# Kernel tuning notes

Measured on AMD Instinct MI355X. Metric: run time of the kernel, lower is better.

The kernel has to match this reference:

```python
import jax, jax.numpy as jnp
import numpy as np

B, T, C, H = 16, 2048, 192, 64

def setup_inputs() -> dict:
    key = jax.random.key(0)
    k1, k2, k3, k4 = jax.random.split(key, 4)
    x = jax.random.normal(k1, (B, T, C), dtype=jnp.float32)
    Wq = jax.random.normal(k2, (C, H), dtype=jnp.float32) * (C ** -0.5)
    Wk = jax.random.normal(k3, (C, H), dtype=jnp.float32) * (C ** -0.5)
    Wv = jax.random.normal(k4, (C, H), dtype=jnp.float32) * (C ** -0.5)
    return {"x": x, "Wq": Wq, "Wk": Wk, "Wv": Wv}

def reference(x, Wq, Wk, Wv):
    # One head of causal self-attention (dropout in eval mode / identity).
    q = x @ Wq                       # [B, T, H]
    k = x @ Wk                       # [B, T, H]
    v = x @ Wv                       # [B, T, H]
    scale = q.shape[-1] ** -0.5
    wei = jnp.einsum('bth,bsh->bts', q, k) * scale   # [B, T, T]
    t = wei.shape[-1]
    causal = jnp.tril(jnp.ones((t, t), dtype=bool))  # tril mask
    wei = jnp.where(causal, wei, -jnp.inf)
    wei = jax.nn.softmax(wei, axis=-1)
    out = jnp.einsum('bts,bsh->bth', wei, v)         # [B, T, H]
    return out
```

## Files before the change

kernel.cpp:

```cpp
#include <hip/hip_runtime.h>

#define B 16
#define T 2048
#define C 192
#define H 64

typedef __bf16 bf16x8 __attribute__((ext_vector_type(8)));
typedef __bf16 bf16x4 __attribute__((ext_vector_type(4)));
typedef float  f32x4  __attribute__((ext_vector_type(4)));

#define MFMA(a, b, c) __builtin_amdgcn_mfma_f32_16x16x32_bf16(a, b, c, 0, 0, 0)

#define SM_BIAS 24.0f

__global__ __launch_bounds__(256) void wtrans_kernel(
    const float* __restrict__ Wq, const float* __restrict__ Wk,
    const float* __restrict__ Wv, __bf16* __restrict__ wt)
{
    const int idx = blockIdx.x * 256 + threadIdx.x;
    const int n = idx / C;
    const int k = idx - n * C;
    const float* W = (n < 64) ? Wq : (n < 128) ? Wk : Wv;
    const int nc = n & 63;
    wt[n * C + k] = (__bf16)W[k * H + nc];
}

__global__ __launch_bounds__(256) void qkv_mfma_kernel(
    const float* __restrict__ x, const __bf16* __restrict__ wt,
    __bf16* __restrict__ qb, __bf16* __restrict__ kb, __bf16* __restrict__ vt)
{
    __shared__ __bf16 Ws[2][192][40];
    __shared__ __bf16 tile[64][72];

    const int tid  = threadIdx.x;
    const int w    = tid >> 6;
    const int lid  = tid & 15;
    const int quad = (tid & 63) >> 4;
    const int m0   = blockIdx.x * 64 + w * 16;

    const float* xrow = x + (size_t)(m0 + lid) * C + quad * 8;
    float4 a0[6], a1[6];
    #pragma unroll
    for (int kc = 0; kc < 6; kc++) {
        a0[kc] = *(const float4*)(xrow + kc * 32);
        a1[kc] = *(const float4*)(xrow + kc * 32 + 4);
    }
    bf16x8 af[6];
    #pragma unroll
    for (int kc = 0; kc < 6; kc++) {
        af[kc][0] = (__bf16)a0[kc].x; af[kc][1] = (__bf16)a0[kc].y;
        af[kc][2] = (__bf16)a0[kc].z; af[kc][3] = (__bf16)a0[kc].w;
        af[kc][4] = (__bf16)a1[kc].x; af[kc][5] = (__bf16)a1[kc].y;
        af[kc][6] = (__bf16)a1[kc].z; af[kc][7] = (__bf16)a1[kc].w;
    }

    bf16x8 wpf[3];
    auto prefW = [&](int kc) {
        #pragma unroll
        for (int i = 0; i < 3; i++) {
            const int p = i * 256 + tid;
            wpf[i] = *(const bf16x8*)(wt + (p >> 2) * C + kc * 32 + (p & 3) * 8);
        }
    };

    f32x4 acc[12] = {};
    prefW(0);
    int cur = 0;
    for (int kc = 0; kc < 6; kc++) {
        #pragma unroll
        for (int i = 0; i < 3; i++) {
            const int p = i * 256 + tid;
            *(bf16x8*)&Ws[cur][p >> 2][(p & 3) * 8] = wpf[i];
        }
        __syncthreads();
        if (kc < 5) prefW(kc + 1);
        #pragma unroll
        for (int nt = 0; nt < 12; nt++) {
            const bf16x8 bfr = *(const bf16x8*)&Ws[cur][nt * 16 + lid][quad * 8];
            acc[nt] = MFMA(af[kc], bfr, acc[nt]);
        }
        cur ^= 1;
    }

    #pragma unroll
    for (int nt = 0; nt < 8; nt++) {
        const int n = nt * 16 + lid;
        __bf16* dst = (n < 64) ? qb : kb;
        const int col = n & 63;
        const float scale = (n < 64) ? 0.1803368801111204f : 1.0f;
        #pragma unroll
        for (int r = 0; r < 4; r++) {
            const int row = m0 + quad * 4 + r;
            dst[(size_t)row * H + col] = (__bf16)(acc[nt][r] * scale);
        }
    }

    #pragma unroll
    for (int nt = 8; nt < 12; nt++) {
        const int col = (nt - 8) * 16 + lid;
        #pragma unroll
        for (int r = 0; r < 4; r++)
            tile[w * 16 + quad * 4 + r][col] = (__bf16)(acc[nt][r]);
    }
    __syncthreads();

    const int bb = blockIdx.x >> 5;
    const int t0 = (blockIdx.x & 31) << 6;
    #pragma unroll
    for (int it = 0; it < 2; ++it) {
        const int h   = it * 32 + (tid >> 3);
        const int tl0 = (tid & 7) * 8;
        bf16x8 d;
        #pragma unroll
        for (int j = 0; j < 8; j++) d[j] = tile[tl0 + j][h];
        *(bf16x8*)(vt + ((size_t)(bb * H + h)) * T + t0 + tl0) = d;
    }
}

__global__ __launch_bounds__(512, 2) void attn_kernel(
    const __bf16* __restrict__ qb,
    const __bf16* __restrict__ kb,
    const __bf16* __restrict__ vt,
    float* __restrict__ out)
{
    __shared__ __bf16 Kb[2][2][64][72];
    __shared__ __bf16 Vb[2][2][64][68];

    const int tid  = threadIdx.x;
    const int wv   = tid >> 6;
    const int grp  = wv >> 2;
    const int w    = wv & 3;
    const int lid  = tid & 15;
    const int quad = (tid & 63) >> 4;

    const int b   = blockIdx.x & 15;
    const int pr  = blockIdx.x >> 4;
    const int qtH = 31 - pr, qtL = pr;
    const int nchH = qtH + 1;
    const int ntot = 33;
    const size_t bbase = (size_t)b * T;

    const int qH = (qtH << 6) + w * 16;
    const int qL = (qtL << 6) + w * 16;

    const __bf16* qrH = qb + (bbase + qH + lid) * H + quad * 8;
    const bf16x8 qfH0 = *(const bf16x8*)(qrH);
    const bf16x8 qfH1 = *(const bf16x8*)(qrH + 32);
    const __bf16* qrL = qb + (bbase + qL + lid) * H + quad * 8;
    const bf16x8 qfL0 = *(const bf16x8*)(qrL);
    const bf16x8 qfL1 = *(const bf16x8*)(qrL + 32);

    const __bf16* kgb = kb + bbase * H;
    const __bf16* vgb = vt + (size_t)b * H * T;

    const int ra = tid >> 3, ca = (tid & 7) * 8;

    auto keyof = [&](int i) {
        if (i > ntot - 1) i = ntot - 1;
        return (i < nchH ? i : i - nchH) << 6;
    };

    bf16x8 kr[2], vr2[2];
    auto prefetch = [&](int s) {
        #pragma unroll
        for (int g = 0; g < 2; g++) {
            const int key0 = keyof(2 * s + g);
            kr[g]  = *(const bf16x8*)(kgb + (size_t)(key0 + ra) * H + ca);
            vr2[g] = *(const bf16x8*)(vgb + (size_t)ra * T + key0 + ca);
        }
    };

    f32x4 OH[4] = {}, OL[4] = {};
    float lsH = 0.f, lsL = 0.f;

    auto doChunk = [&](f32x4 (&O)[4], float& ls, bf16x8 cq0, bf16x8 cq1,
                       int cqw, int key0, int cur) {
        const __bf16 (*Kc)[72] = Kb[cur][grp];
        const __bf16 (*Vc)[68] = Vb[cur][grp];
        bf16x8 kf[8];
        #pragma unroll
        for (int j = 0; j < 4; j++) {
            kf[2*j]   = *(const bf16x8*)&Kc[j * 16 + lid][quad * 8];
            kf[2*j+1] = *(const bf16x8*)&Kc[j * 16 + lid][32 + quad * 8];
        }
        bf16x8 bv0[4], bv1[4];
        #pragma unroll
        for (int ht = 0; ht < 4; ht++) {
            const __bf16* vr_ = &Vc[ht * 16 + lid][quad * 4];
            ((bf16x4*)&bv0[ht])[0] = *(const bf16x4*)(vr_);
            ((bf16x4*)&bv0[ht])[1] = *(const bf16x4*)(vr_ + 16);
            ((bf16x4*)&bv1[ht])[0] = *(const bf16x4*)(vr_ + 32);
            ((bf16x4*)&bv1[ht])[1] = *(const bf16x4*)(vr_ + 48);
        }
        bf16x8 af0, af1;
        const bool boundary = (key0 + 63 > cqw);
        #pragma unroll
        for (int j = 0; j < 4; j++) {
            f32x4 sS = {-SM_BIAS, -SM_BIAS, -SM_BIAS, -SM_BIAS};
            sS = MFMA(kf[2*j], cq0, sS);
            sS = MFMA(kf[2*j+1], cq1, sS);
            if (boundary) {
                #pragma unroll
                for (int r = 0; r < 4; r++)
                    if (key0 + j * 16 + quad * 4 + r > cqw + lid) sS[r] = -1e30f;
            }
            #pragma unroll
            for (int r = 0; r < 4; r++) {
                const float p = __builtin_amdgcn_exp2f(sS[r]);
                ls += p;
                if      (j == 0) af0[r]     = (__bf16)p;
                else if (j == 1) af0[4 + r] = (__bf16)p;
                else if (j == 2) af1[r]     = (__bf16)p;
                else             af1[4 + r] = (__bf16)p;
            }
        }
        #pragma unroll
        for (int ht = 0; ht < 4; ht++) {
            O[ht] = MFMA(af0, bv0[ht], O[ht]);
            O[ht] = MFMA(af1, bv1[ht], O[ht]);
        }
    };

    prefetch(0);
    int cur = 0;
    for (int s = 0; s < 17; s++) {
        *(bf16x8*)&Kb[cur][0][ra][ca] = kr[0];
        *(bf16x8*)&Kb[cur][1][ra][ca] = kr[1];
        *(bf16x8*)&Vb[cur][0][ra][ca] = vr2[0];
        *(bf16x8*)&Vb[cur][1][ra][ca] = vr2[1];
        __syncthreads();
        if (s + 1 < 17) prefetch(s + 1);

        const int i = 2 * s + grp;
        if (i < ntot) {
            const bool heavy = (i < nchH);
            const int key0 = (heavy ? i : i - nchH) << 6;
            if (heavy) doChunk(OH, lsH, qfH0, qfH1, qH, key0, cur);
            else       doChunk(OL, lsL, qfL0, qfL1, qL, key0, cur);
        }
        cur ^= 1;
    }

    __syncthreads();
    float* sO = (float*)&Kb[0][0][0][0];
    float* sL = (float*)&Vb[0][0][0][0];

    float lh = lsH; lh += __shfl_xor(lh, 16, 64); lh += __shfl_xor(lh, 32, 64);
    float ll = lsL; ll += __shfl_xor(ll, 16, 64); ll += __shfl_xor(ll, 32, 64);

    if (grp == 1) {
        #pragma unroll
        for (int ht = 0; ht < 4; ht++)
            #pragma unroll
            for (int r = 0; r < 4; r++) {
                sO[((0 * 4 + w) * 16 + quad * 4 + r) * 64 + ht * 16 + lid] = OH[ht][r];
                sO[((1 * 4 + w) * 16 + quad * 4 + r) * 64 + ht * 16 + lid] = OL[ht][r];
            }
        if ((tid & 63) < 16) {
            sL[(0 * 4 + w) * 16 + lid] = lh;
            sL[(1 * 4 + w) * 16 + lid] = ll;
        }
    }
    __syncthreads();
    if (grp == 0) {
        lh += sL[(0 * 4 + w) * 16 + lid];
        ll += sL[(1 * 4 + w) * 16 + lid];
        #pragma unroll
        for (int ht = 0; ht < 4; ht++)
            #pragma unroll
            for (int r = 0; r < 4; r++) {
                const float LrH = __shfl(lh, quad * 4 + r, 16);
                const float vH = OH[ht][r]
                    + sO[((0 * 4 + w) * 16 + quad * 4 + r) * 64 + ht * 16 + lid];
                out[(bbase + qH + quad * 4 + r) * H + ht * 16 + lid] = vH / LrH;

                const float LrL = __shfl(ll, quad * 4 + r, 16);
                const float vL = OL[ht][r]
                    + sO[((1 * 4 + w) * 16 + quad * 4 + r) * 64 + ht * 16 + lid];
                out[(bbase + qL + quad * 4 + r) * H + ht * 16 + lid] = vL / LrL;
            }
    }
}

extern "C" void kernel_launch(void* const* d_in, const int* in_sizes, int n_in,
                              void* d_out, int out_size, void* d_ws, size_t ws_size,
                              hipStream_t stream)
{
    const float* x  = (const float*)d_in[0];
    const float* Wq = (const float*)d_in[1];
    const float* Wk = (const float*)d_in[2];
    const float* Wv = (const float*)d_in[3];

    const size_t BTH = (size_t)B * T * H;
    __bf16* qbuf = (__bf16*)d_ws;
    __bf16* kbuf = qbuf + BTH;
    __bf16* vtb  = kbuf + BTH;
    __bf16* wt   = vtb + BTH;
    float* outp = (float*)d_out;

    wtrans_kernel<<<(C * 3 * H) / 256, 256, 0, stream>>>(Wq, Wk, Wv, wt);
    qkv_mfma_kernel<<<B * T / 64, 256, 0, stream>>>(x, wt, qbuf, kbuf, vtb);
    attn_kernel<<<B * T / 128, 512, 0, stream>>>(qbuf, kbuf, vtb, outp);
}
```

Baseline: 105.7 us.

## Split QKV projection into 32-row blocks with 2x2 wave layout

The QKV projection kernel now handles 32 rows per block instead of 64. Its four waves form a 2x2 grid over rows and output columns, so each wave holds 6 accumulators instead of 12. This doubles the grid size and cuts register and LDS use, which should raise occupancy and spread the projection across more CUs. The cost is single-buffered weight tiles with an extra barrier per k-step, and every x row block now reloads the full weight matrix.

```diff
diff --git a/kernel.cpp b/kernel.cpp
--- a/kernel.cpp
+++ b/kernel.cpp
@@ -25,33 +25,31 @@
     wt[n * C + k] = (__bf16)W[k * H + nc];
 }
 
-__global__ __launch_bounds__(256) void qkv_mfma_kernel(
+__global__ __launch_bounds__(256, 4) void qkv_mfma_kernel(
     const float* __restrict__ x, const __bf16* __restrict__ wt,
     __bf16* __restrict__ qb, __bf16* __restrict__ kb, __bf16* __restrict__ vt)
 {
-    __shared__ __bf16 Ws[2][192][40];
-    __shared__ __bf16 tile[64][72];
+    __shared__ __bf16 Ws[192][40];
+    __shared__ __bf16 tile[32][72];
 
     const int tid  = threadIdx.x;
     const int w    = tid >> 6;
+    const int rw   = w & 1;
+    const int cw   = w >> 1;
     const int lid  = tid & 15;
     const int quad = (tid & 63) >> 4;
-    const int m0   = blockIdx.x * 64 + w * 16;
+    const int m0   = blockIdx.x * 32 + rw * 16;
 
     const float* xrow = x + (size_t)(m0 + lid) * C + quad * 8;
-    float4 a0[6], a1[6];
-    #pragma unroll
-    for (int kc = 0; kc < 6; kc++) {
-        a0[kc] = *(const float4*)(xrow + kc * 32);
-        a1[kc] = *(const float4*)(xrow + kc * 32 + 4);
-    }
     bf16x8 af[6];
     #pragma unroll
     for (int kc = 0; kc < 6; kc++) {
-        af[kc][0] = (__bf16)a0[kc].x; af[kc][1] = (__bf16)a0[kc].y;
-        af[kc][2] = (__bf16)a0[kc].z; af[kc][3] = (__bf16)a0[kc].w;
-        af[kc][4] = (__bf16)a1[kc].x; af[kc][5] = (__bf16)a1[kc].y;
-        af[kc][6] = (__bf16)a1[kc].z; af[kc][7] = (__bf16)a1[kc].w;
+        const float4 a0 = *(const float4*)(xrow + kc * 32);
+        const float4 a1 = *(const float4*)(xrow + kc * 32 + 4);
+        af[kc][0] = (__bf16)a0.x; af[kc][1] = (__bf16)a0.y;
+        af[kc][2] = (__bf16)a0.z; af[kc][3] = (__bf16)a0.w;
+        af[kc][4] = (__bf16)a1.x; af[kc][5] = (__bf16)a1.y;
+        af[kc][6] = (__bf16)a1.z; af[kc][7] = (__bf16)a1.w;
     }
 
     bf16x8 wpf[3];
@@ -63,58 +61,54 @@
         }
     };
 
-    f32x4 acc[12] = {};
+    f32x4 acc[6] = {};
     prefW(0);
-    int cur = 0;
     for (int kc = 0; kc < 6; kc++) {
         #pragma unroll
         for (int i = 0; i < 3; i++) {
             const int p = i * 256 + tid;
-            *(bf16x8*)&Ws[cur][p >> 2][(p & 3) * 8] = wpf[i];
+            *(bf16x8*)&Ws[p >> 2][(p & 3) * 8] = wpf[i];
         }
         __syncthreads();
         if (kc < 5) prefW(kc + 1);
         #pragma unroll
-        for (int nt = 0; nt < 12; nt++) {
-            const bf16x8 bfr = *(const bf16x8*)&Ws[cur][nt * 16 + lid][quad * 8];
-            acc[nt] = MFMA(af[kc], bfr, acc[nt]);
-        }
-        cur ^= 1;
+        for (int j = 0; j < 6; j++) {
+            const int nt = cw * 6 + j;
+            const bf16x8 bfr = *(const bf16x8*)&Ws[nt * 16 + lid][quad * 8];
+            acc[j] = MFMA(af[kc], bfr, acc[j]);
+        }
+        __syncthreads();
     }
 
     #pragma unroll
-    for (int nt = 0; nt < 8; nt++) {
-        const int n = nt * 16 + lid;
-        __bf16* dst = (n < 64) ? qb : kb;
-        const int col = n & 63;
-        const float scale = (n < 64) ? 0.1803368801111204f : 1.0f;
-        #pragma unroll
-        for (int r = 0; r < 4; r++) {
-            const int row = m0 + quad * 4 + r;
-            dst[(size_t)row * H + col] = (__bf16)(acc[nt][r] * scale);
-        }
-    }
-
+    for (int j = 0; j < 6; j++) {
+        const int nt = cw * 6 + j;
+        const int n  = nt * 16 + lid;
+        if (n < 128) {
+            __bf16* dst = (n < 64) ? qb : kb;
+            const int col = n & 63;
+            const float scale = (n < 64) ? 0.1803368801111204f : 1.0f;
+            #pragma unroll
+            for (int r = 0; r < 4; r++)
+                dst[(size_t)(m0 + quad * 4 + r) * H + col] =
+                    (__bf16)(acc[j][r] * scale);
+        } else {
+            const int col = n - 128;
+            #pragma unroll
+            for (int r = 0; r < 4; r++)
+                tile[rw * 16 + quad * 4 + r][col] = (__bf16)acc[j][r];
+        }
+    }
+    __syncthreads();
+
+    const int bb  = blockIdx.x >> 6;
+    const int t0  = (blockIdx.x & 63) << 5;
+    const int h   = tid >> 2;
+    const int tl0 = (tid & 3) * 8;
+    bf16x8 d;
     #pragma unroll
-    for (int nt = 8; nt < 12; nt++) {
-        const int col = (nt - 8) * 16 + lid;
-        #pragma unroll
-        for (int r = 0; r < 4; r++)
-            tile[w * 16 + quad * 4 + r][col] = (__bf16)(acc[nt][r]);
-    }
-    __syncthreads();
-
-    const int bb = blockIdx.x >> 5;
-    const int t0 = (blockIdx.x & 31) << 6;
-    #pragma unroll
-    for (int it = 0; it < 2; ++it) {
-        const int h   = it * 32 + (tid >> 3);
-        const int tl0 = (tid & 7) * 8;
-        bf16x8 d;
-        #pragma unroll
-        for (int j = 0; j < 8; j++) d[j] = tile[tl0 + j][h];
-        *(bf16x8*)(vt + ((size_t)(bb * H + h)) * T + t0 + tl0) = d;
-    }
+    for (int j = 0; j < 8; j++) d[j] = tile[tl0 + j][h];
+    *(bf16x8*)(vt + ((size_t)(bb * H + h)) * T + t0 + tl0) = d;
 }
 
 __global__ __launch_bounds__(512, 2) void attn_kernel(
@@ -299,6 +293,6 @@
     float* outp = (float*)d_out;
 
     wtrans_kernel<<<(C * 3 * H) / 256, 256, 0, stream>>>(Wq, Wk, Wv, wt);
-    qkv_mfma_kernel<<<B * T / 64, 256, 0, stream>>>(x, wt, qbuf, kbuf, vtb);
+    qkv_mfma_kernel<<<B * T / 32, 256, 0, stream>>>(x, wt, qbuf, kbuf, vtb);
     attn_kernel<<<B * T / 128, 512, 0, stream>>>(qbuf, kbuf, vtb, outp);
 }
```

New measurement: 109.5 us. 1.04x slower.

## Split attention key chunks across four wave groups in 1024-thread blocks

Applied to the files above, without the earlier changes.

Raises the attention block from 512 to 1024 threads, so four wave groups each take one 64-key chunk per step instead of two groups. This cuts the loop from 17 steps to 9 and widens the cross-group reduction of partial outputs and row sums to three extra groups through shared memory. K and V fragments are now loaded from LDS inside the MFMA loops instead of all up front, which lowers register pressure. In exchange the kernel uses more LDS per block, adds a bigger reduction at the end, and still pays a block-wide barrier each step.

```diff
diff --git a/kernel.cpp b/kernel.cpp
--- a/kernel.cpp
+++ b/kernel.cpp
@@ -117,14 +117,16 @@
     }
 }
 
-__global__ __launch_bounds__(512, 2) void attn_kernel(
+#define KB_ELEMS (64 * 72)
+#define VB_ELEMS (64 * 68)
+
+__global__ __launch_bounds__(1024) void attn_kernel(
     const __bf16* __restrict__ qb,
     const __bf16* __restrict__ kb,
     const __bf16* __restrict__ vt,
     float* __restrict__ out)
 {
-    __shared__ __bf16 Kb[2][2][64][72];
-    __shared__ __bf16 Vb[2][2][64][68];
+    __shared__ __align__(16) __bf16 smem[8 * KB_ELEMS + 8 * VB_ELEMS];
 
     const int tid  = threadIdx.x;
     const int wv   = tid >> 6;
@@ -138,7 +140,15 @@
     const int qtH = 31 - pr, qtL = pr;
     const int nchH = qtH + 1;
     const int ntot = 33;
+    const int nsteps = 9;
     const size_t bbase = (size_t)b * T;
+
+    auto Kbp = [&](int cu, int c) -> __bf16 (*)[72] {
+        return (__bf16(*)[72])(smem + (cu * 4 + c) * KB_ELEMS);
+    };
+    auto Vbp = [&](int cu, int c) -> __bf16 (*)[68] {
+        return (__bf16(*)[68])(smem + 8 * KB_ELEMS + (cu * 4 + c) * VB_ELEMS);
+    };
 
     const int qH = (qtH << 6) + w * 16;
     const int qL = (qtL << 6) + w * 16;
@@ -153,7 +163,9 @@
     const __bf16* kgb = kb + bbase * H;
     const __bf16* vgb = vt + (size_t)b * H * T;
 
-    const int ra = tid >> 3, ca = (tid & 7) * 8;
+    const int g2 = tid >> 9;
+    const int tt = tid & 511;
+    const int ra = tt >> 3, ca = (tt & 7) * 8;
 
     auto keyof = [&](int i) {
         if (i > ntot - 1) i = ntot - 1;
@@ -163,10 +175,10 @@
     bf16x8 kr[2], vr2[2];
     auto prefetch = [&](int s) {
         #pragma unroll
-        for (int g = 0; g < 2; g++) {
-            const int key0 = keyof(2 * s + g);
-            kr[g]  = *(const bf16x8*)(kgb + (size_t)(key0 + ra) * H + ca);
-            vr2[g] = *(const bf16x8*)(vgb + (size_t)ra * T + key0 + ca);
+        for (int u = 0; u < 2; u++) {
+            const int key0 = keyof(4 * s + 2 * g2 + u);
+            kr[u]  = *(const bf16x8*)(kgb + (size_t)(key0 + ra) * H + ca);
+            vr2[u] = *(const bf16x8*)(vgb + (size_t)ra * T + key0 + ca);
         }
     };
 
@@ -175,30 +187,17 @@
 
     auto doChunk = [&](f32x4 (&O)[4], float& ls, bf16x8 cq0, bf16x8 cq1,
                        int cqw, int key0, int cur) {
-        const __bf16 (*Kc)[72] = Kb[cur][grp];
-        const __bf16 (*Vc)[68] = Vb[cur][grp];
-        bf16x8 kf[8];
-        #pragma unroll
-        for (int j = 0; j < 4; j++) {
-            kf[2*j]   = *(const bf16x8*)&Kc[j * 16 + lid][quad * 8];
-            kf[2*j+1] = *(const bf16x8*)&Kc[j * 16 + lid][32 + quad * 8];
-        }
-        bf16x8 bv0[4], bv1[4];
-        #pragma unroll
-        for (int ht = 0; ht < 4; ht++) {
-            const __bf16* vr_ = &Vc[ht * 16 + lid][quad * 4];
-            ((bf16x4*)&bv0[ht])[0] = *(const bf16x4*)(vr_);
-            ((bf16x4*)&bv0[ht])[1] = *(const bf16x4*)(vr_ + 16);
-            ((bf16x4*)&bv1[ht])[0] = *(const bf16x4*)(vr_ + 32);
-            ((bf16x4*)&bv1[ht])[1] = *(const bf16x4*)(vr_ + 48);
-        }
+        const __bf16 (*Kc)[72] = Kbp(cur, grp);
+        const __bf16 (*Vc)[68] = Vbp(cur, grp);
         bf16x8 af0, af1;
         const bool boundary = (key0 + 63 > cqw);
         #pragma unroll
         for (int j = 0; j < 4; j++) {
+            const bf16x8 k0 = *(const bf16x8*)&Kc[j * 16 + lid][quad * 8];
+            const bf16x8 k1 = *(const bf16x8*)&Kc[j * 16 + lid][32 + quad * 8];
             f32x4 sS = {-SM_BIAS, -SM_BIAS, -SM_BIAS, -SM_BIAS};
-            sS = MFMA(kf[2*j], cq0, sS);
-            sS = MFMA(kf[2*j+1], cq1, sS);
+            sS = MFMA(k0, cq0, sS);
+            sS = MFMA(k1, cq1, sS);
             if (boundary) {
                 #pragma unroll
                 for (int r = 0; r < 4; r++)
@@ -216,22 +215,30 @@
         }
         #pragma unroll
         for (int ht = 0; ht < 4; ht++) {
-            O[ht] = MFMA(af0, bv0[ht], O[ht]);
-            O[ht] = MFMA(af1, bv1[ht], O[ht]);
+            const __bf16* vr_ = &Vc[ht * 16 + lid][quad * 4];
+            bf16x8 bv0, bv1;
+            ((bf16x4*)&bv0)[0] = *(const bf16x4*)(vr_);
+            ((bf16x4*)&bv0)[1] = *(const bf16x4*)(vr_ + 16);
+            ((bf16x4*)&bv1)[0] = *(const bf16x4*)(vr_ + 32);
+            ((bf16x4*)&bv1)[1] = *(const bf16x4*)(vr_ + 48);
+            O[ht] = MFMA(af0, bv0, O[ht]);
+            O[ht] = MFMA(af1, bv1, O[ht]);
         }
     };
 
     prefetch(0);
     int cur = 0;
-    for (int s = 0; s < 17; s++) {
-        *(bf16x8*)&Kb[cur][0][ra][ca] = kr[0];
-        *(bf16x8*)&Kb[cur][1][ra][ca] = kr[1];
-        *(bf16x8*)&Vb[cur][0][ra][ca] = vr2[0];
-        *(bf16x8*)&Vb[cur][1][ra][ca] = vr2[1];
+    for (int s = 0; s < nsteps; s++) {
+        #pragma unroll
+        for (int u = 0; u < 2; u++) {
+            const int c = 2 * g2 + u;
+            *(bf16x8*)&Kbp(cur, c)[ra][ca] = kr[u];
+            *(bf16x8*)&Vbp(cur, c)[ra][ca] = vr2[u];
+        }
         __syncthreads();
-        if (s + 1 < 17) prefetch(s + 1);
-
-        const int i = 2 * s + grp;
+        if (s + 1 < nsteps) prefetch(s + 1);
+
+        const int i = 4 * s + grp;
         if (i < ntot) {
             const bool heavy = (i < nchH);
             const int key0 = (heavy ? i : i - nchH) << 6;
@@ -242,41 +249,46 @@
     }
 
     __syncthreads();
-    float* sO = (float*)&Kb[0][0][0][0];
-    float* sL = (float*)&Vb[0][0][0][0];
+    float* sO = (float*)smem;
+    float* sL = sO + 3 * 8192;
 
     float lh = lsH; lh += __shfl_xor(lh, 16, 64); lh += __shfl_xor(lh, 32, 64);
     float ll = lsL; ll += __shfl_xor(ll, 16, 64); ll += __shfl_xor(ll, 32, 64);
 
-    if (grp == 1) {
+    if (grp != 0) {
+        const int gg = grp - 1;
         #pragma unroll
         for (int ht = 0; ht < 4; ht++)
             #pragma unroll
             for (int r = 0; r < 4; r++) {
-                sO[((0 * 4 + w) * 16 + quad * 4 + r) * 64 + ht * 16 + lid] = OH[ht][r];
-                sO[((1 * 4 + w) * 16 + quad * 4 + r) * 64 + ht * 16 + lid] = OL[ht][r];
+                sO[((gg * 2 + 0) * 4 + w) * 1024 + (quad * 4 + r) * 64 + ht * 16 + lid] = OH[ht][r];
+                sO[((gg * 2 + 1) * 4 + w) * 1024 + (quad * 4 + r) * 64 + ht * 16 + lid] = OL[ht][r];
             }
         if ((tid & 63) < 16) {
-            sL[(0 * 4 + w) * 16 + lid] = lh;
-            sL[(1 * 4 + w) * 16 + lid] = ll;
+            sL[gg * 128 +      w * 16 + lid] = lh;
+            sL[gg * 128 + 64 + w * 16 + lid] = ll;
         }
     }
     __syncthreads();
     if (grp == 0) {
-        lh += sL[(0 * 4 + w) * 16 + lid];
-        ll += sL[(1 * 4 + w) * 16 + lid];
+        #pragma unroll
+        for (int gg = 0; gg < 3; gg++) {
+            lh += sL[gg * 128 +      w * 16 + lid];
+            ll += sL[gg * 128 + 64 + w * 16 + lid];
+        }
         #pragma unroll
         for (int ht = 0; ht < 4; ht++)
             #pragma unroll
             for (int r = 0; r < 4; r++) {
+                float vH = OH[ht][r], vL = OL[ht][r];
+                #pragma unroll
+                for (int gg = 0; gg < 3; gg++) {
+                    vH += sO[((gg * 2 + 0) * 4 + w) * 1024 + (quad * 4 + r) * 64 + ht * 16 + lid];
+                    vL += sO[((gg * 2 + 1) * 4 + w) * 1024 + (quad * 4 + r) * 64 + ht * 16 + lid];
+                }
                 const float LrH = __shfl(lh, quad * 4 + r, 16);
-                const float vH = OH[ht][r]
-                    + sO[((0 * 4 + w) * 16 + quad * 4 + r) * 64 + ht * 16 + lid];
+                const float LrL = __shfl(ll, quad * 4 + r, 16);
                 out[(bbase + qH + quad * 4 + r) * H + ht * 16 + lid] = vH / LrH;
-
-                const float LrL = __shfl(ll, quad * 4 + r, 16);
-                const float vL = OL[ht][r]
-                    + sO[((1 * 4 + w) * 16 + quad * 4 + r) * 64 + ht * 16 + lid];
                 out[(bbase + qL + quad * 4 + r) * H + ht * 16 + lid] = vL / LrL;
             }
     }
@@ -300,5 +312,5 @@
 
     wtrans_kernel<<<(C * 3 * H) / 256, 256, 0, stream>>>(Wq, Wk, Wv, wt);
     qkv_mfma_kernel<<<B * T / 64, 256, 0, stream>>>(x, wt, qbuf, kbuf, vtb);
-    attn_kernel<<<B * T / 128, 512, 0, stream>>>(qbuf, kbuf, vtb, outp);
+    attn_kernel<<<B * T / 128, 1024, 0, stream>>>(qbuf, kbuf, vtb, outp);
 }
```

Measured after the change: 106.9 us. About the same (+1.2%).

## Fuse weight transpose into QKV projection kernel and enlarge block to 128 rows

Applied to the files above, without the earlier changes.

Drops the separate weight-transpose kernel. Each QKV block now reads the fp32 Wq/Wk/Wv directly, converts them to bf16 and transposes them into shared memory. Blocks grow to 512 threads covering 128 rows, so the weight-loading cost is spread over more rows. This removes one kernel launch and the workspace round trip, but every block now reloads all of W and does scalar transposed LDS stores, which may cause bank conflicts.

```diff
diff --git a/kernel.cpp b/kernel.cpp
--- a/kernel.cpp
+++ b/kernel.cpp
@@ -13,74 +13,59 @@
 
 #define SM_BIAS 24.0f
 
-__global__ __launch_bounds__(256) void wtrans_kernel(
+__global__ __launch_bounds__(512) void qkv_mfma_kernel(
+    const float* __restrict__ x,
     const float* __restrict__ Wq, const float* __restrict__ Wk,
-    const float* __restrict__ Wv, __bf16* __restrict__ wt)
-{
-    const int idx = blockIdx.x * 256 + threadIdx.x;
-    const int n = idx / C;
-    const int k = idx - n * C;
-    const float* W = (n < 64) ? Wq : (n < 128) ? Wk : Wv;
-    const int nc = n & 63;
-    wt[n * C + k] = (__bf16)W[k * H + nc];
-}
-
-__global__ __launch_bounds__(256) void qkv_mfma_kernel(
-    const float* __restrict__ x, const __bf16* __restrict__ wt,
+    const float* __restrict__ Wv,
     __bf16* __restrict__ qb, __bf16* __restrict__ kb, __bf16* __restrict__ vt)
 {
-    __shared__ __bf16 Ws[2][192][40];
-    __shared__ __bf16 tile[64][72];
+    __shared__ __bf16 Ws[192][200];
+    __shared__ __bf16 tile[128][72];
 
     const int tid  = threadIdx.x;
     const int w    = tid >> 6;
     const int lid  = tid & 15;
     const int quad = (tid & 63) >> 4;
-    const int m0   = blockIdx.x * 64 + w * 16;
+    const int m0   = blockIdx.x * 128 + w * 16;
+
+    #pragma unroll
+    for (int i = 0; i < 18; i++) {
+        const int p = i * 512 + tid;
+        const int m = p / 3072;
+        const int r = p - m * 3072;
+        const int k = r >> 4;
+        const int nc4 = (r & 15) << 2;
+        const float* W = (m == 0) ? Wq : (m == 1) ? Wk : Wv;
+        const float4 v = *(const float4*)(W + k * H + nc4);
+        const int n = m * 64 + nc4;
+        Ws[n + 0][k] = (__bf16)v.x;
+        Ws[n + 1][k] = (__bf16)v.y;
+        Ws[n + 2][k] = (__bf16)v.z;
+        Ws[n + 3][k] = (__bf16)v.w;
+    }
 
     const float* xrow = x + (size_t)(m0 + lid) * C + quad * 8;
-    float4 a0[6], a1[6];
+    bf16x8 af[6];
     #pragma unroll
     for (int kc = 0; kc < 6; kc++) {
-        a0[kc] = *(const float4*)(xrow + kc * 32);
-        a1[kc] = *(const float4*)(xrow + kc * 32 + 4);
-    }
-    bf16x8 af[6];
-    #pragma unroll
-    for (int kc = 0; kc < 6; kc++) {
-        af[kc][0] = (__bf16)a0[kc].x; af[kc][1] = (__bf16)a0[kc].y;
-        af[kc][2] = (__bf16)a0[kc].z; af[kc][3] = (__bf16)a0[kc].w;
-        af[kc][4] = (__bf16)a1[kc].x; af[kc][5] = (__bf16)a1[kc].y;
-        af[kc][6] = (__bf16)a1[kc].z; af[kc][7] = (__bf16)a1[kc].w;
-    }
-
-    bf16x8 wpf[3];
-    auto prefW = [&](int kc) {
-        #pragma unroll
-        for (int i = 0; i < 3; i++) {
-            const int p = i * 256 + tid;
-            wpf[i] = *(const bf16x8*)(wt + (p >> 2) * C + kc * 32 + (p & 3) * 8);
-        }
-    };
+        const float4 a0 = *(const float4*)(xrow + kc * 32);
+        const float4 a1 = *(const float4*)(xrow + kc * 32 + 4);
+        af[kc][0] = (__bf16)a0.x; af[kc][1] = (__bf16)a0.y;
+        af[kc][2] = (__bf16)a0.z; af[kc][3] = (__bf16)a0.w;
+        af[kc][4] = (__bf16)a1.x; af[kc][5] = (__bf16)a1.y;
+        af[kc][6] = (__bf16)a1.z; af[kc][7] = (__bf16)a1.w;
+    }
+    __syncthreads();
 
     f32x4 acc[12] = {};
-    prefW(0);
-    int cur = 0;
-    for (int kc = 0; kc < 6; kc++) {
-        #pragma unroll
-        for (int i = 0; i < 3; i++) {
-            const int p = i * 256 + tid;
-            *(bf16x8*)&Ws[cur][p >> 2][(p & 3) * 8] = wpf[i];
-        }
-        __syncthreads();
-        if (kc < 5) prefW(kc + 1);
+    #pragma unroll
+    for (int kc = 0; kc < 6; kc++)
         #pragma unroll
         for (int nt = 0; nt < 12; nt++) {
-            const bf16x8 bfr = *(const bf16x8*)&Ws[cur][nt * 16 + lid][quad * 8];
+            const bf16x8 bfr =
+                *(const bf16x8*)&Ws[nt * 16 + lid][kc * 32 + quad * 8];
             acc[nt] = MFMA(af[kc], bfr, acc[nt]);
         }
-        cur ^= 1;
-    }
 
     #pragma unroll
     for (int nt = 0; nt < 8; nt++) {
@@ -104,12 +89,13 @@
     }
     __syncthreads();
 
-    const int bb = blockIdx.x >> 5;
-    const int t0 = (blockIdx.x & 31) << 6;
+    const int bb = blockIdx.x >> 4;
+    const int t0 = (blockIdx.x & 15) << 7;
     #pragma unroll
     for (int it = 0; it < 2; ++it) {
-        const int h   = it * 32 + (tid >> 3);
-        const int tl0 = (tid & 7) * 8;
+        const int q   = it * 512 + tid;
+        const int h   = q >> 4;
+        const int tl0 = (q & 15) * 8;
         bf16x8 d;
         #pragma unroll
         for (int j = 0; j < 8; j++) d[j] = tile[tl0 + j][h];
@@ -295,10 +281,9 @@
     __bf16* qbuf = (__bf16*)d_ws;
     __bf16* kbuf = qbuf + BTH;
     __bf16* vtb  = kbuf + BTH;
-    __bf16* wt   = vtb + BTH;
     float* outp = (float*)d_out;
 
-    wtrans_kernel<<<(C * 3 * H) / 256, 256, 0, stream>>>(Wq, Wk, Wv, wt);
-    qkv_mfma_kernel<<<B * T / 64, 256, 0, stream>>>(x, wt, qbuf, kbuf, vtb);
+    qkv_mfma_kernel<<<B * T / 128, 512, 0, stream>>>(x, Wq, Wk, Wv,
+                                                     qbuf, kbuf, vtb);
     attn_kernel<<<B * T / 128, 512, 0, stream>>>(qbuf, kbuf, vtb, outp);
 }
```

Result: no change. 103.8 us (-1.7%).
